# Performance work log

Hardware: AMD Instinct MI355X
Metric: run time of the kernel (lower is better)

## Reference

```python
import jax, jax.numpy as jnp
import numpy as np
from jax import lax

B, T, I, H = 64, 512, 128, 512
ALPHA = 0.1  # dt/tau = 10/100


def setup_inputs() -> dict:
    key = jax.random.key(0)
    k1, k2, k3 = jax.random.split(key, 3)
    return {
        "x": jax.random.normal(k1, (B, T, I), dtype=jnp.float32),
        "init_state": jnp.zeros((B, H), dtype=jnp.float32),
        "W_in": jax.random.normal(k2, (H, I), dtype=jnp.float32) / np.sqrt(I),
        "b_in": jnp.zeros((H,), dtype=jnp.float32),
        "W_hid": jax.random.normal(k3, (H, H), dtype=jnp.float32) / np.sqrt(H),
        "b_hid": jnp.zeros((H,), dtype=jnp.float32),
        "alpha": jnp.full((H,), ALPHA, dtype=jnp.float32),
    }


def reference(x, init_state, W_in, b_in, W_hid, b_hid, alpha):
    # x: [B, T, I] -> outputs: ([B, T, H], [B, T, H])
    fr0 = jax.nn.relu(init_state)

    def step(carry, u_t):
        fr, v = carry                       # [B, H] each
        v_in = u_t @ W_in.T + b_in          # input Linear
        v_hid = fr @ W_hid.T + b_hid        # hidden Linear
        v_new = (1.0 - alpha) * v + alpha * (v_hid + v_in)   # leaky integration
        v_r = (1.0 - alpha) * v_new + alpha * v_hid          # relaxed state
        fr_new = jax.nn.relu(v_new)
        fr_r = jax.nn.relu(v_r)
        return (fr_new, v_new), (fr_new, fr_r)

    xs = jnp.swapaxes(x, 0, 1)  # [T, B, I]
    _, (states, relax_states) = lax.scan(step, (fr0, init_state), xs)
    return jnp.swapaxes(states, 0, 1), jnp.swapaxes(relax_states, 0, 1)
```

## Files before the change

### kernel.cpp

```cpp
#include <hip/hip_runtime.h>
#include <hip/hip_fp16.h>

#define B_ 64
#define T_ 512
#define I_ 128
#define H_ 512

typedef _Float16 half2v __attribute__((ext_vector_type(2)));

__device__ __forceinline__ float dot2(unsigned a, unsigned b, float c) {
    return __builtin_amdgcn_fdot2(__builtin_bit_cast(half2v, a),
                                  __builtin_bit_cast(half2v, b), c, false);
}

__device__ __forceinline__ unsigned short f32_to_f16b(float f) {
    _Float16 h = (_Float16)f;
    return __builtin_bit_cast(unsigned short, h);
}

__global__ void wconv(const float* __restrict__ Whid,
                      unsigned* __restrict__ Wz) {
    int p = blockIdx.x * 256 + threadIdx.x;
    int m  = p & 3;
    int u4 = p >> 2;
    int l, g, w, i;
    if (u4 < 24576) {
        l = u4 & 63; g = (u4 >> 6) & 7;
        int r = u4 >> 9;
        w = r / 6; i = r - 6 * w;
    } else {
        int q = u4 - 24576;
        l = q & 63; g = (q >> 6) & 7;
        int r = q >> 9;
        w = r >> 1; i = 6 + (r & 1);
    }
    int h  = l + 64 * i;
    int kp = 32 * w + 4 * g + m;
    float w0 = Whid[h * H_ + 2 * kp];
    float w1 = Whid[h * H_ + 2 * kp + 1];
    half2v hw = { (_Float16)w0, (_Float16)w1 };
    Wz[p] = __builtin_bit_cast(unsigned, hw);
}

__global__ __launch_bounds__(256) void vin_gemm(const float* __restrict__ x,
                                                const float* __restrict__ Win,
                                                const float* __restrict__ bin,
                                                float* __restrict__ vin) {
    __shared__ __align__(16) unsigned xs[64 * 64];
    __shared__ __align__(16) unsigned ws[64 * 64];
    const int tid = threadIdx.x;
    const int m0 = blockIdx.x * 64;
    const int n0 = blockIdx.y * 64;

    #pragma unroll
    for (int r = 0; r < 8; ++r) {
        int gi = r * 256 + tid;
        int row = gi >> 5;
        int c4 = gi & 31;
        float4 vx = ((const float4*)(x + (size_t)(m0 + row) * I_))[c4];
        float4 vw = ((const float4*)(Win + (size_t)(n0 + row) * I_))[c4];
        int sw = (row >> 2) & 15;
        int col = 4 * ((c4 >> 1) ^ sw) + (c4 & 1) * 2;
        half2v x01 = { (_Float16)vx.x, (_Float16)vx.y };
        half2v x23 = { (_Float16)vx.z, (_Float16)vx.w };
        half2v w01 = { (_Float16)vw.x, (_Float16)vw.y };
        half2v w23 = { (_Float16)vw.z, (_Float16)vw.w };
        xs[row * 64 + col]     = __builtin_bit_cast(unsigned, x01);
        xs[row * 64 + col + 1] = __builtin_bit_cast(unsigned, x23);
        ws[row * 64 + col]     = __builtin_bit_cast(unsigned, w01);
        ws[row * 64 + col + 1] = __builtin_bit_cast(unsigned, w23);
    }
    __syncthreads();

    const int ty = tid >> 4, tx = tid & 15;
    float acc[4][4] = {};
    #pragma unroll
    for (int kb = 0; kb < 16; ++kb) {
        uint4 a4[4], b4[4];
        #pragma unroll
        for (int i = 0; i < 4; ++i)
            a4[i] = *(const uint4*)&xs[(ty * 4 + i) * 64 + 4 * (kb ^ ty)];
        #pragma unroll
        for (int j = 0; j < 4; ++j)
            b4[j] = *(const uint4*)&ws[(tx * 4 + j) * 64 + 4 * (kb ^ tx)];
        #pragma unroll
        for (int i = 0; i < 4; ++i)
            #pragma unroll
            for (int j = 0; j < 4; ++j) {
                acc[i][j] = dot2(a4[i].x, b4[j].x, acc[i][j]);
                acc[i][j] = dot2(a4[i].y, b4[j].y, acc[i][j]);
                acc[i][j] = dot2(a4[i].z, b4[j].z, acc[i][j]);
                acc[i][j] = dot2(a4[i].w, b4[j].w, acc[i][j]);
            }
    }

    float4 bv = ((const float4*)(bin + n0))[tx];
    #pragma unroll
    for (int i = 0; i < 4; ++i) {
        int m = m0 + ty * 4 + i;
        float4 o;
        o.x = acc[i][0] + bv.x; o.y = acc[i][1] + bv.y;
        o.z = acc[i][2] + bv.z; o.w = acc[i][3] + bv.w;
        ((float4*)(vin + (size_t)m * H_ + n0))[tx] = o;
    }
}

__global__ __launch_bounds__(512, 2)
__attribute__((amdgpu_waves_per_eu(2, 2)))
void recurrent(
        const uint4* __restrict__ Wz4,
        const float* __restrict__ vin,
        const float* __restrict__ init_state,
        const float* __restrict__ b_hid,
        const float* __restrict__ alpha,
        float* __restrict__ out0,
        float* __restrict__ out1) {
    __shared__ uint4 ldsW[8192];
    __shared__ uint4 frbuf4[2][64];
    __shared__ float pbuf[8][640];

    const int t = threadIdx.x;
    const int b = blockIdx.x;
    const int w = t >> 6, l = t & 63;

    uint4 wv[6][8];
    const uint4* wp = Wz4 + (size_t)(w * 48) * 64 + l;
    #pragma unroll
    for (int i = 0; i < 6; ++i)
        #pragma unroll
        for (int g = 0; g < 8; ++g)
            wv[i][g] = wp[(i * 8 + g) * 64];
    #pragma unroll
    for (int i = 0; i < 6; ++i)
        #pragma unroll
        for (int g = 0; g < 8; ++g)
            asm volatile("" : "+v"(wv[i][g].x), "+v"(wv[i][g].y),
                              "+v"(wv[i][g].z), "+v"(wv[i][g].w));

    const uint4* lsrc = Wz4 + 24576;
    #pragma unroll
    for (int kk = 0; kk < 16; ++kk) ldsW[kk * 512 + t] = lsrc[kk * 512 + t];

    unsigned short* fr16 = (unsigned short*)frbuf4;
    float v = init_state[b * H_ + t];
    fr16[t] = f32_to_f16b(fmaxf(v, 0.0f));
    const float bh = b_hid[t];
    const float al = alpha[t];
    const float om = 1.0f - al;

    const float* vinp = vin + (size_t)b * T_ * H_ + t;
    float* o0 = out0 + (size_t)b * T_ * H_ + t;
    float* o1 = out1 + (size_t)b * T_ * H_ + t;

    const int lw0 = (w * 2) * 8 * 64 + l;
    float* prow = &pbuf[w][l * 10];

    __syncthreads();

    for (int s = 0; s < T_; ++s) {
        const int par = s & 1;
        float vinv = vinp[(size_t)s * H_];

        const uint4* fb = &frbuf4[par][w * 8];
        float a0 = 0.f, a1 = 0.f, a2 = 0.f, a3 = 0.f;
        float a4 = 0.f, a5 = 0.f, a6 = 0.f, a7 = 0.f;

        #pragma unroll
        for (int g = 0; g < 8; ++g) {
            uint4 wl0 = ldsW[lw0 + g * 64];
            uint4 wl1 = ldsW[lw0 + 512 + g * 64];
            uint4 f = fb[g];
            a0 = dot2(f.x, wv[0][g].x, a0); a0 = dot2(f.y, wv[0][g].y, a0);
            a0 = dot2(f.z, wv[0][g].z, a0); a0 = dot2(f.w, wv[0][g].w, a0);
            a1 = dot2(f.x, wv[1][g].x, a1); a1 = dot2(f.y, wv[1][g].y, a1);
            a1 = dot2(f.z, wv[1][g].z, a1); a1 = dot2(f.w, wv[1][g].w, a1);
            a2 = dot2(f.x, wv[2][g].x, a2); a2 = dot2(f.y, wv[2][g].y, a2);
            a2 = dot2(f.z, wv[2][g].z, a2); a2 = dot2(f.w, wv[2][g].w, a2);
            a3 = dot2(f.x, wv[3][g].x, a3); a3 = dot2(f.y, wv[3][g].y, a3);
            a3 = dot2(f.z, wv[3][g].z, a3); a3 = dot2(f.w, wv[3][g].w, a3);
            a4 = dot2(f.x, wv[4][g].x, a4); a4 = dot2(f.y, wv[4][g].y, a4);
            a4 = dot2(f.z, wv[4][g].z, a4); a4 = dot2(f.w, wv[4][g].w, a4);
            a5 = dot2(f.x, wv[5][g].x, a5); a5 = dot2(f.y, wv[5][g].y, a5);
            a5 = dot2(f.z, wv[5][g].z, a5); a5 = dot2(f.w, wv[5][g].w, a5);
            a6 = dot2(f.x, wl0.x, a6); a6 = dot2(f.y, wl0.y, a6);
            a6 = dot2(f.z, wl0.z, a6); a6 = dot2(f.w, wl0.w, a6);
            a7 = dot2(f.x, wl1.x, a7); a7 = dot2(f.y, wl1.y, a7);
            a7 = dot2(f.z, wl1.z, a7); a7 = dot2(f.w, wl1.w, a7);
        }

        float2* pr = (float2*)prow;
        pr[0] = make_float2(a0, a1);
        pr[1] = make_float2(a2, a3);
        pr[2] = make_float2(a4, a5);
        pr[3] = make_float2(a6, a7);

        asm volatile("s_waitcnt lgkmcnt(0)" ::: "memory");
        __builtin_amdgcn_s_barrier();

        float sum = pbuf[0][l * 10 + w] + pbuf[1][l * 10 + w]
                  + pbuf[2][l * 10 + w] + pbuf[3][l * 10 + w]
                  + pbuf[4][l * 10 + w] + pbuf[5][l * 10 + w]
                  + pbuf[6][l * 10 + w] + pbuf[7][l * 10 + w];

        float vhid = sum + bh;
        float vnew = om * v + al * (vhid + vinv);
        float vr   = om * vnew + al * vhid;
        v = vnew;
        float frn = fmaxf(vnew, 0.0f);
        float frr = fmaxf(vr, 0.0f);

        o0[(size_t)s * H_] = frn;
        o1[(size_t)s * H_] = frr;
        fr16[(par ^ 1) * 512 + t] = f32_to_f16b(frn);

        asm volatile("s_waitcnt lgkmcnt(0)" ::: "memory");
        __builtin_amdgcn_s_barrier();
    }
}

extern "C" void kernel_launch(void* const* d_in, const int* in_sizes, int n_in,
                              void* d_out, int out_size, void* d_ws, size_t ws_size,
                              hipStream_t stream) {
    const float* x          = (const float*)d_in[0];
    const float* init_state = (const float*)d_in[1];
    const float* W_in       = (const float*)d_in[2];
    const float* b_in       = (const float*)d_in[3];
    const float* W_hid      = (const float*)d_in[4];
    const float* b_hid      = (const float*)d_in[5];
    const float* alpha      = (const float*)d_in[6];

    float* out0 = (float*)d_out;
    float* out1 = out0 + (size_t)B_ * T_ * H_;

    char* ws = (char*)d_ws;
    float*    vin = (float*)ws;
    unsigned* Wz  = (unsigned*)(ws + 67108864);

    hipLaunchKernelGGL(wconv, dim3(512), dim3(256), 0, stream,
                       W_hid, Wz);
    hipLaunchKernelGGL(vin_gemm, dim3(512, 8), dim3(256), 0, stream,
                       x, W_in, b_in, vin);
    hipLaunchKernelGGL(recurrent, dim3(64), dim3(512), 0, stream,
                       (const uint4*)Wz, vin, init_state, b_hid, alpha,
                       out0, out1);
}
```

Measured before the change: 922.5 us.

## Compute recurrent hidden matvec with MFMA and partition output columns per wave

Result: slower. 1.035 ms (+12.2%).

```diff
diff --git a/kernel.cpp b/kernel.cpp
--- a/kernel.cpp
+++ b/kernel.cpp
@@ -7,6 +7,8 @@
 #define H_ 512
 
 typedef _Float16 half2v __attribute__((ext_vector_type(2)));
+typedef _Float16 f16x8  __attribute__((ext_vector_type(8)));
+typedef float    f32x4  __attribute__((ext_vector_type(4)));
 
 __device__ __forceinline__ float dot2(unsigned a, unsigned b, float c) {
     return __builtin_amdgcn_fdot2(__builtin_bit_cast(half2v, a),
@@ -17,27 +19,23 @@
     _Float16 h = (_Float16)f;
     return __builtin_bit_cast(unsigned short, h);
 }
+
+#define MFMA(ACC, A, Bq) \
+    ACC = __builtin_amdgcn_mfma_f32_16x16x32_f16((A), (Bq), (ACC), 0, 0, 0)
 
 __global__ void wconv(const float* __restrict__ Whid,
                       unsigned* __restrict__ Wz) {
     int p = blockIdx.x * 256 + threadIdx.x;
     int m  = p & 3;
     int u4 = p >> 2;
-    int l, g, w, i;
-    if (u4 < 24576) {
-        l = u4 & 63; g = (u4 >> 6) & 7;
-        int r = u4 >> 9;
-        w = r / 6; i = r - 6 * w;
-    } else {
-        int q = u4 - 24576;
-        l = q & 63; g = (q >> 6) & 7;
-        int r = q >> 9;
-        w = r >> 1; i = 6 + (r & 1);
-    }
-    int h  = l + 64 * i;
-    int kp = 32 * w + 4 * g + m;
-    float w0 = Whid[h * H_ + 2 * kp];
-    float w1 = Whid[h * H_ + 2 * kp + 1];
+    int l  = u4 & 63;
+    int nt = (u4 >> 6) & 3;
+    int kt = (u4 >> 8) & 15;
+    int w  = (u4 >> 12) & 7;
+    int h  = 64 * w + 16 * nt + (l & 15);
+    int k  = 32 * kt + 8 * (l >> 4) + 2 * m;
+    float w0 = Whid[h * H_ + k];
+    float w1 = Whid[h * H_ + k + 1];
     half2v hw = { (_Float16)w0, (_Float16)w1 };
     Wz[p] = __builtin_bit_cast(unsigned, hw);
 }
@@ -115,103 +113,104 @@
         const float* __restrict__ alpha,
         float* __restrict__ out0,
         float* __restrict__ out1) {
-    __shared__ uint4 ldsW[8192];
-    __shared__ uint4 frbuf4[2][64];
-    __shared__ float pbuf[8][640];
+    __shared__ uint4 ldsWb[8192];
+    __shared__ unsigned short fr16[2][512];
 
     const int t = threadIdx.x;
     const int b = blockIdx.x;
     const int w = t >> 6, l = t & 63;
-
-    uint4 wv[6][8];
-    const uint4* wp = Wz4 + (size_t)(w * 48) * 64 + l;
-    #pragma unroll
-    for (int i = 0; i < 6; ++i)
-        #pragma unroll
-        for (int g = 0; g < 8; ++g)
-            wv[i][g] = wp[(i * 8 + g) * 64];
-    #pragma unroll
-    for (int i = 0; i < 6; ++i)
-        #pragma unroll
-        for (int g = 0; g < 8; ++g)
-            asm volatile("" : "+v"(wv[i][g].x), "+v"(wv[i][g].y),
-                              "+v"(wv[i][g].z), "+v"(wv[i][g].w));
-
-    const uint4* lsrc = Wz4 + 24576;
-    #pragma unroll
-    for (int kk = 0; kk < 16; ++kk) ldsW[kk * 512 + t] = lsrc[kk * 512 + t];
-
-    unsigned short* fr16 = (unsigned short*)frbuf4;
+    const int hi = l >> 4;
+
+    const uint4* wbase = Wz4 + (size_t)w * 4096 + l;
+
+    f16x8 wb[10][4];
+    #pragma unroll
+    for (int kt = 0; kt < 10; ++kt)
+        #pragma unroll
+        for (int nt = 0; nt < 4; ++nt) {
+            uint4 u = wbase[(kt * 4 + nt) * 64];
+            wb[kt][nt] = __builtin_bit_cast(f16x8, u);
+            asm("" : "+a"(wb[kt][nt]));
+        }
+
+    #pragma unroll
+    for (int i = 0; i < 16; ++i)
+        ldsWb[w * 1024 + i * 64 + l] = wbase[2560 + i * 64];
+
+    const uint4* gp = wbase + 3584;
+
     float v = init_state[b * H_ + t];
-    fr16[t] = f32_to_f16b(fmaxf(v, 0.0f));
+    fr16[0][t] = f32_to_f16b(fmaxf(v, 0.0f));
     const float bh = b_hid[t];
     const float al = alpha[t];
     const float om = 1.0f - al;
+    const bool sel4 = (l & 16) != 0;
+    const bool sel5 = (l & 32) != 0;
 
     const float* vinp = vin + (size_t)b * T_ * H_ + t;
     float* o0 = out0 + (size_t)b * T_ * H_ + t;
     float* o1 = out1 + (size_t)b * T_ * H_ + t;
 
-    const int lw0 = (w * 2) * 8 * 64 + l;
-    float* prow = &pbuf[w][l * 10];
-
     __syncthreads();
 
     for (int s = 0; s < T_; ++s) {
         const int par = s & 1;
+
+        asm volatile("" : "+v"(gp));
+        uint4 g0 = gp[0],   g1 = gp[64],  g2 = gp[128], g3 = gp[192];
+        uint4 g4 = gp[256], g5 = gp[320], g6 = gp[384], g7 = gp[448];
         float vinv = vinp[(size_t)s * H_];
 
-        const uint4* fb = &frbuf4[par][w * 8];
-        float a0 = 0.f, a1 = 0.f, a2 = 0.f, a3 = 0.f;
-        float a4 = 0.f, a5 = 0.f, a6 = 0.f, a7 = 0.f;
-
-        #pragma unroll
-        for (int g = 0; g < 8; ++g) {
-            uint4 wl0 = ldsW[lw0 + g * 64];
-            uint4 wl1 = ldsW[lw0 + 512 + g * 64];
-            uint4 f = fb[g];
-            a0 = dot2(f.x, wv[0][g].x, a0); a0 = dot2(f.y, wv[0][g].y, a0);
-            a0 = dot2(f.z, wv[0][g].z, a0); a0 = dot2(f.w, wv[0][g].w, a0);
-            a1 = dot2(f.x, wv[1][g].x, a1); a1 = dot2(f.y, wv[1][g].y, a1);
-            a1 = dot2(f.z, wv[1][g].z, a1); a1 = dot2(f.w, wv[1][g].w, a1);
-            a2 = dot2(f.x, wv[2][g].x, a2); a2 = dot2(f.y, wv[2][g].y, a2);
-            a2 = dot2(f.z, wv[2][g].z, a2); a2 = dot2(f.w, wv[2][g].w, a2);
-            a3 = dot2(f.x, wv[3][g].x, a3); a3 = dot2(f.y, wv[3][g].y, a3);
-            a3 = dot2(f.z, wv[3][g].z, a3); a3 = dot2(f.w, wv[3][g].w, a3);
-            a4 = dot2(f.x, wv[4][g].x, a4); a4 = dot2(f.y, wv[4][g].y, a4);
-            a4 = dot2(f.z, wv[4][g].z, a4); a4 = dot2(f.w, wv[4][g].w, a4);
-            a5 = dot2(f.x, wv[5][g].x, a5); a5 = dot2(f.y, wv[5][g].y, a5);
-            a5 = dot2(f.z, wv[5][g].z, a5); a5 = dot2(f.w, wv[5][g].w, a5);
-            a6 = dot2(f.x, wl0.x, a6); a6 = dot2(f.y, wl0.y, a6);
-            a6 = dot2(f.z, wl0.z, a6); a6 = dot2(f.w, wl0.w, a6);
-            a7 = dot2(f.x, wl1.x, a7); a7 = dot2(f.y, wl1.y, a7);
-            a7 = dot2(f.z, wl1.z, a7); a7 = dot2(f.w, wl1.w, a7);
-        }
-
-        float2* pr = (float2*)prow;
-        pr[0] = make_float2(a0, a1);
-        pr[1] = make_float2(a2, a3);
-        pr[2] = make_float2(a4, a5);
-        pr[3] = make_float2(a6, a7);
-
-        asm volatile("s_waitcnt lgkmcnt(0)" ::: "memory");
-        __builtin_amdgcn_s_barrier();
-
-        float sum = pbuf[0][l * 10 + w] + pbuf[1][l * 10 + w]
-                  + pbuf[2][l * 10 + w] + pbuf[3][l * 10 + w]
-                  + pbuf[4][l * 10 + w] + pbuf[5][l * 10 + w]
-                  + pbuf[6][l * 10 + w] + pbuf[7][l * 10 + w];
-
-        float vhid = sum + bh;
+        f32x4 acc0 = {0.f, 0.f, 0.f, 0.f}, acc1 = {0.f, 0.f, 0.f, 0.f};
+        f32x4 acc2 = {0.f, 0.f, 0.f, 0.f}, acc3 = {0.f, 0.f, 0.f, 0.f};
+
+        const f16x8* frb =
+            (const f16x8*)((const char*)&fr16[par][0] + hi * 16);
+
+        #pragma unroll
+        for (int kt = 0; kt < 10; ++kt) {
+            f16x8 afr = frb[kt * 4];
+            MFMA(acc0, afr, wb[kt][0]);
+            MFMA(acc1, afr, wb[kt][1]);
+            MFMA(acc2, afr, wb[kt][2]);
+            MFMA(acc3, afr, wb[kt][3]);
+        }
+        #pragma unroll
+        for (int kt = 10; kt < 14; ++kt) {
+            f16x8 afr = frb[kt * 4];
+            const f16x8* lb =
+                (const f16x8*)&ldsWb[w * 1024 + (kt - 10) * 256 + l];
+            MFMA(acc0, afr, lb[0]);
+            MFMA(acc1, afr, lb[64]);
+            MFMA(acc2, afr, lb[128]);
+            MFMA(acc3, afr, lb[192]);
+        }
+        {
+            f16x8 a14 = frb[14 * 4];
+            MFMA(acc0, a14, __builtin_bit_cast(f16x8, g0));
+            MFMA(acc1, a14, __builtin_bit_cast(f16x8, g1));
+            MFMA(acc2, a14, __builtin_bit_cast(f16x8, g2));
+            MFMA(acc3, a14, __builtin_bit_cast(f16x8, g3));
+            f16x8 a15 = frb[15 * 4];
+            MFMA(acc0, a15, __builtin_bit_cast(f16x8, g4));
+            MFMA(acc1, a15, __builtin_bit_cast(f16x8, g5));
+            MFMA(acc2, a15, __builtin_bit_cast(f16x8, g6));
+            MFMA(acc3, a15, __builtin_bit_cast(f16x8, g7));
+        }
+
+        float s01 = sel4 ? acc1.x : acc0.x;
+        float s23 = sel4 ? acc3.x : acc2.x;
+        float vh  = sel5 ? s23 : s01;
+
+        float vhid = vh + bh;
         float vnew = om * v + al * (vhid + vinv);
-        float vr   = om * vnew + al * vhid;
+        float frn  = fmaxf(vnew, 0.0f);
+        fr16[par ^ 1][t] = f32_to_f16b(frn);
+        float vr = om * vnew + al * vhid;
         v = vnew;
-        float frn = fmaxf(vnew, 0.0f);
         float frr = fmaxf(vr, 0.0f);
-
         o0[(size_t)s * H_] = frn;
         o1[(size_t)s * H_] = frr;
-        fr16[(par ^ 1) * 512 + t] = f32_to_f16b(frn);
 
         asm volatile("s_waitcnt lgkmcnt(0)" ::: "memory");
         __builtin_amdgcn_s_barrier();
```
